# Kernel optimization log

Hardware: AMD Instinct MI355X
Metric: run time of the kernel (lower is better)

Reference implementation:

```python
import jax, jax.numpy as jnp
import numpy as np

BS, LX, LY, D, H, DK = 2, 2048, 2048, 1024, 16, 64


def setup_inputs() -> dict:
    key = jax.random.key(0)
    ks = jax.random.split(key, 12)
    s = 1.0 / np.sqrt(D)
    return {
        "x": jax.random.normal(ks[0], (BS, LX, D), jnp.float32),
        "y": jax.random.normal(ks[1], (BS, LY, D), jnp.float32),
        "mask": jnp.zeros((BS, 1, LX, LY), jnp.float32),
        "Wq": jax.random.normal(ks[2], (D, H * DK), jnp.float32) * s,
        "bq": jnp.zeros((H * DK,), jnp.float32),
        "Wk": jax.random.normal(ks[3], (D, H * DK), jnp.float32) * s,
        "bk": jnp.zeros((H * DK,), jnp.float32),
        "Wv": jax.random.normal(ks[4], (D, H * DK), jnp.float32) * s,
        "bv": jnp.zeros((H * DK,), jnp.float32),
        "Wo": jax.random.normal(ks[5], (H * DK, D), jnp.float32) * s,
        "bo": jnp.zeros((D,), jnp.float32),
    }


def reference(x, y, mask, Wq, bq, Wk, bk, Wv, bv, Wo, bo):
    bs, lx, _ = x.shape
    ly = y.shape[1]
    norm = DK ** 0.5
    # projections -> (bs, len, H, DK)
    q = (x @ Wq + bq).reshape(bs, lx, H, DK)
    k = (y @ Wk + bk).reshape(bs, ly, H, DK)
    v = (y @ Wv + bv).reshape(bs, ly, H, DK)
    # scores: (bs, H, lx, ly)
    scores = jnp.einsum('bxhd,byhd->bhxy', q, k) / norm + mask
    attn = jax.nn.softmax(scores, axis=-1)
    # output: (bs, lx, H, DK) -> (bs, lx, H*DK)
    out = jnp.einsum('bhxy,byhd->bxhd', attn, v).reshape(bs, lx, H * DK)
    return out @ Wo + bo
```

## Files before the change

kernel.cpp:

```cpp
#include <hip/hip_runtime.h>
#include <hip/hip_bf16.h>


typedef __bf16 bf16;
typedef __bf16 bf16x4 __attribute__((ext_vector_type(4)));
typedef __bf16 bf16x8 __attribute__((ext_vector_type(8)));
typedef float floatx4 __attribute__((ext_vector_type(4)));

#define MFMA16(a, b, c) __builtin_amdgcn_mfma_f32_16x16x32_bf16(a, b, c, 0, 0, 0)

constexpr int BS = 2, LX = 2048, LY = 2048, D = 1024, H = 16, DK = 64;
constexpr int HD = H * DK;
constexpr float LOG2E = 1.4426950408889634f;

__device__ __forceinline__ void cp16(const bf16* g, bf16* l) {
  __builtin_amdgcn_global_load_lds(
      (const __attribute__((address_space(1))) unsigned int*)g,
      (__attribute__((address_space(3))) unsigned int*)l, 16, 0, 0);
}

__global__ __launch_bounds__(256) void prep(const float* __restrict__ W0, bf16* __restrict__ T0,
                                            const float* __restrict__ W1, bf16* __restrict__ T1,
                                            const float* __restrict__ W2, bf16* __restrict__ T2,
                                            const float* __restrict__ W3, bf16* __restrict__ T3,
                                            const float* __restrict__ x, bf16* __restrict__ xb,
                                            const float* __restrict__ y, bf16* __restrict__ yb,
                                            const float* __restrict__ mask, int* __restrict__ flags) {
  const int id = blockIdx.x;
  const int t = threadIdx.x;
  if (id < 1024) {
    __shared__ bf16 tile[64][72];
    const float* W;
    bf16* T;
    switch (id >> 8) {
      case 0: W = W0; T = T0; break;
      case 1: W = W1; T = T1; break;
      case 2: W = W2; T = T2; break;
      default: W = W3; T = T3; break;
    }
    const int kt = id & 15, nt = (id >> 4) & 15;
    const int r = t >> 2, c4 = (t & 3) * 16;
    const float* src = W + (size_t)(kt * 64 + r) * 1024 + nt * 64 + c4;
#pragma unroll
    for (int i = 0; i < 16; i++) tile[r][c4 + i] = (bf16)src[i];
    __syncthreads();
    bf16 vals[16];
#pragma unroll
    for (int i = 0; i < 16; i++) vals[i] = tile[c4 + i][r];
    bf16* dst = T + (size_t)(nt * 64 + r) * 1024 + kt * 64 + c4;
#pragma unroll
    for (int i = 0; i < 16; i++) dst[i] = vals[i];
  } else if (id < 5120) {
    const int id2 = id - 1024;
    const float* src = (id2 >= 2048) ? y : x;
    bf16* dst = (id2 >= 2048) ? yb : xb;
    const size_t i = ((size_t)(id2 & 2047) * 256 + t) * 8;
    float4 a = *(const float4*)(src + i);
    float4 c = *(const float4*)(src + i + 4);
    bf16 tmp[8] = {(bf16)a.x, (bf16)a.y, (bf16)a.z, (bf16)a.w,
                   (bf16)c.x, (bf16)c.y, (bf16)c.z, (bf16)c.w};
    *(bf16x8*)(dst + i) = *(const bf16x8*)tmp;
  } else {
    const int id3 = id - 5120;
    const int region = id3 >> 5, sub = id3 & 31;
    const float4* p = (const float4*)mask + (size_t)region * 65536 + sub * 2048;
    bool nz = false;
#pragma unroll
    for (int it = 0; it < 8; it++) {
      float4 v = p[it * 256 + t];
      nz |= (v.x != 0.f) | (v.y != 0.f) | (v.z != 0.f) | (v.w != 0.f);
    }
    if (nz) atomicOr(&flags[region], 1);
  }
}

__global__ __launch_bounds__(512, 2) void qkv8(const bf16* __restrict__ xb, const bf16* __restrict__ yb,
                                               const bf16* __restrict__ Wtq, const bf16* __restrict__ Wtk,
                                               const bf16* __restrict__ Wtv,
                                               const float* __restrict__ bq, const float* __restrict__ bk,
                                               const float* __restrict__ bv,
                                               bf16* __restrict__ Qb, bf16* __restrict__ Kb,
                                               bf16* __restrict__ Vt) {
  constexpr int K = 1024, N = 1024;
  __shared__ __align__(16) bf16 As[2][2][128 * 64];
  __shared__ __align__(16) bf16 Bs[2][2][128 * 64];

  const int z = blockIdx.z;
  const bf16* A = (z == 0) ? xb : yb;
  const bf16* Bt = (z == 0) ? Wtq : (z == 1) ? Wtk : Wtv;
  const float* bias = (z == 0) ? bq : (z == 1) ? bk : bv;

  const int t = threadIdx.x;
  const int w = t >> 6, lane = t & 63, quad = lane >> 4, l15 = lane & 15;
  const int wm = w >> 2, wn = w & 3;
  const int mbase = blockIdx.y * 256, nbase = blockIdx.x * 256;
  const int srow = lane >> 3, schunk = (lane & 7) ^ srow;
  const int sx = quad ^ (l15 & 7);

  floatx4 acc[2][4][2][2] = {};
  bf16x8 af[4][2];
  bf16x8 bfr[2][2][2];

#define ST_A(ktt, half, slot)                                                                 \
  {                                                                                           \
    _Pragma("unroll") for (int j = 0; j < 2; j++) {                                           \
      const int r0 = w * 16 + j * 8;                                                          \
      cp16(A + (size_t)(mbase + (half) * 128 + r0 + srow) * K + (ktt) * 64 + schunk * 8,      \
           &As[slot][half][r0 * 64]);                                                         \
    }                                                                                         \
  }
#define ST_B(ktt, half, slot)                                                                 \
  {                                                                                           \
    _Pragma("unroll") for (int j = 0; j < 2; j++) {                                           \
      const int r0 = w * 16 + j * 8;                                                          \
      cp16(Bt + (size_t)(nbase + (half) * 128 + r0 + srow) * K + (ktt) * 64 + schunk * 8,     \
           &Bs[slot][half][r0 * 64]);                                                         \
    }                                                                                         \
  }
#define LOAD_A(slot, mh)                                                                      \
  {                                                                                           \
    _Pragma("unroll") for (int i = 0; i < 4; i++) {                                           \
      const bf16* p = &As[slot][mh][(wm * 64 + i * 16 + l15) * 64];                           \
      af[i][0] = *(const bf16x8*)(p + sx * 8);                                                \
      af[i][1] = *(const bf16x8*)(p + (sx ^ 4) * 8);                                          \
    }                                                                                         \
  }
#define LOAD_B(slot, nh)                                                                      \
  {                                                                                           \
    _Pragma("unroll") for (int j = 0; j < 2; j++) {                                           \
      const bf16* p = &Bs[slot][nh][(wn * 32 + j * 16 + l15) * 64];                           \
      bfr[nh][j][0] = *(const bf16x8*)(p + sx * 8);                                           \
      bfr[nh][j][1] = *(const bf16x8*)(p + (sx ^ 4) * 8);                                     \
    }                                                                                         \
  }
#define MFMA_Q(mh, nh)                                                                        \
  {                                                                                           \
    _Pragma("unroll") for (int i = 0; i < 4; i++)                                             \
        _Pragma("unroll") for (int j = 0; j < 2; j++) {                                       \
      acc[mh][i][nh][j] = MFMA16(af[i][0], bfr[nh][j][0], acc[mh][i][nh][j]);                 \
      acc[mh][i][nh][j] = MFMA16(af[i][1], bfr[nh][j][1], acc[mh][i][nh][j]);                 \
    }                                                                                         \
  }
#define BARX()                       \
  {                                  \
    asm volatile("" ::: "memory");   \
    __builtin_amdgcn_s_barrier();    \
    asm volatile("" ::: "memory");   \
  }
#define VMW(n) asm volatile("s_waitcnt vmcnt(" #n ")" ::: "memory")
#define LG0() asm volatile("s_waitcnt lgkmcnt(0)" ::: "memory")
#define NOPST {}
#define TILE_BODY(PAR, STG0, V0, STG1, V1, STG2, STG3, V3)  \
  {                                                         \
    LOAD_A(PAR, 0);                                         \
    LOAD_B(PAR, 0);                                         \
    STG0;                                                   \
    V0;                                                     \
    BARX();                                                 \
    LG0();                                                  \
    __builtin_amdgcn_s_setprio(1);                          \
    MFMA_Q(0, 0);                                           \
    __builtin_amdgcn_s_setprio(0);                          \
    BARX();                                                 \
    LOAD_B(PAR, 1);                                         \
    STG1;                                                   \
    V1;                                                     \
    BARX();                                                 \
    LG0();                                                  \
    __builtin_amdgcn_s_setprio(1);                          \
    MFMA_Q(0, 1);                                           \
    __builtin_amdgcn_s_setprio(0);                          \
    BARX();                                                 \
    LOAD_A(PAR, 1);                                         \
    STG2;                                                   \
    BARX();                                                 \
    LG0();                                                  \
    __builtin_amdgcn_s_setprio(1);                          \
    MFMA_Q(1, 0);                                           \
    __builtin_amdgcn_s_setprio(0);                          \
    BARX();                                                 \
    STG3;                                                   \
    V3;                                                     \
    BARX();                                                 \
    LG0();                                                  \
    __builtin_amdgcn_s_setprio(1);                          \
    MFMA_Q(1, 1);                                           \
    __builtin_amdgcn_s_setprio(0);                          \
    BARX();                                                 \
  }

  ST_A(0, 0, 0);
  ST_B(0, 0, 0);
  ST_B(0, 1, 0);
  ST_A(0, 1, 0);
  ST_A(1, 0, 1);
  ST_B(1, 0, 1);
  VMW(8);
  BARX();

#pragma unroll 1
  for (int kt = 0; kt < 14; kt += 2) {
    TILE_BODY(0, ST_B(kt + 1, 1, 1), VMW(8), ST_A(kt + 1, 1, 1), VMW(8),
              ST_A(kt + 2, 0, 0), ST_B(kt + 2, 0, 0), VMW(8));
    TILE_BODY(1, ST_B(kt + 2, 1, 0), VMW(8), ST_A(kt + 2, 1, 0), VMW(8),
              ST_A(kt + 3, 0, 1), ST_B(kt + 3, 0, 1), VMW(8));
  }
  TILE_BODY(0, ST_B(15, 1, 1), VMW(8), ST_A(15, 1, 1), VMW(8), NOPST, NOPST, VMW(4));
  TILE_BODY(1, NOPST, VMW(2), NOPST, VMW(0), NOPST, NOPST, NOPST);

#undef TILE_BODY
#undef NOPST
#undef LG0
#undef VMW
#undef BARX
#undef MFMA_Q
#undef LOAD_B
#undef LOAD_A
#undef ST_B
#undef ST_A

  if (z <= 1) {
    bf16* outp = (z == 0) ? Qb : Kb;
    const float sc = (z == 0) ? 0.125f * LOG2E : 1.0f;
#pragma unroll
    for (int nh = 0; nh < 2; nh++)
#pragma unroll
      for (int j = 0; j < 2; j++) {
        const int n = nbase + nh * 128 + wn * 32 + j * 16 + l15;
        const float bv2 = bias[n];
#pragma unroll
        for (int mh = 0; mh < 2; mh++)
#pragma unroll
          for (int i = 0; i < 4; i++)
#pragma unroll
            for (int r = 0; r < 4; r++) {
              const int m = mbase + mh * 128 + wm * 64 + i * 16 + quad * 4 + r;
              outp[(size_t)m * N + n] = (bf16)((acc[mh][i][nh][j][r] + bv2) * sc);
            }
      }
  } else {
    const int b = mbase >> 11;
    const int y0 = mbase & 2047;
#pragma unroll
    for (int nh = 0; nh < 2; nh++)
#pragma unroll
      for (int j = 0; j < 2; j++) {
        const int n = nbase + nh * 128 + wn * 32 + j * 16 + l15;
        const float bv2 = bias[n];
        const int hh = n >> 6, dk = n & 63;
        bf16* dst0 = Vt + ((size_t)(b * H + hh) * DK + dk) * LY + y0;
#pragma unroll
        for (int mh = 0; mh < 2; mh++)
#pragma unroll
          for (int i = 0; i < 4; i++) {
            const int yy = mh * 128 + wm * 64 + i * 16 + quad * 4;
            bf16 tmp[4];
#pragma unroll
            for (int r = 0; r < 4; r++) tmp[r] = (bf16)(acc[mh][i][nh][j][r] + bv2);
            *(bf16x4*)(dst0 + yy) = *(const bf16x4*)tmp;
          }
      }
  }
}

__global__ __launch_bounds__(256) void out_gemm(const bf16* __restrict__ A, const bf16* __restrict__ Bt,
                                                const float* __restrict__ bias, float* __restrict__ outp) {
  constexpr int K = 1024, N = 1024;
  __shared__ __align__(16) bf16 As[128 * 64];
  __shared__ __align__(16) bf16 Bs[64 * 64];
  const int t = threadIdx.x;
  const int w = t >> 6, lane = t & 63, quad = lane >> 4, l15 = lane & 15;
  const int mbase = blockIdx.y * 128, nbase = blockIdx.x * 64;
  const int srow = lane >> 3, schunk = (lane & 7) ^ srow;
  const int sx = quad ^ (l15 & 7);

  floatx4 acc[2][4] = {};
  for (int k0 = 0; k0 < K; k0 += 64) {
    __syncthreads();
#pragma unroll
    for (int j = 0; j < 4; j++) {
      const int r0 = w * 32 + j * 8;
      cp16(A + (size_t)(mbase + r0 + srow) * K + k0 + schunk * 8, As + r0 * 64);
    }
#pragma unroll
    for (int j = 0; j < 2; j++) {
      const int r0 = w * 16 + j * 8;
      cp16(Bt + (size_t)(nbase + r0 + srow) * K + k0 + schunk * 8, Bs + r0 * 64);
    }
    __syncthreads();
    bf16x8 af[2][2], bfr[4][2];
#pragma unroll
    for (int i = 0; i < 2; i++) {
      const int ra = w * 32 + i * 16 + l15;
      af[i][0] = *(const bf16x8*)&As[ra * 64 + sx * 8];
      af[i][1] = *(const bf16x8*)&As[ra * 64 + (sx ^ 4) * 8];
    }
#pragma unroll
    for (int jn = 0; jn < 4; jn++) {
      const int rb = jn * 16 + l15;
      bfr[jn][0] = *(const bf16x8*)&Bs[rb * 64 + sx * 8];
      bfr[jn][1] = *(const bf16x8*)&Bs[rb * 64 + (sx ^ 4) * 8];
    }
#pragma unroll
    for (int i = 0; i < 2; i++)
#pragma unroll
      for (int jn = 0; jn < 4; jn++) {
        acc[i][jn] = MFMA16(af[i][0], bfr[jn][0], acc[i][jn]);
        acc[i][jn] = MFMA16(af[i][1], bfr[jn][1], acc[i][jn]);
      }
  }
#pragma unroll
  for (int jn = 0; jn < 4; jn++) {
    const int n = nbase + jn * 16 + l15;
    const float bv2 = bias[n];
#pragma unroll
    for (int i = 0; i < 2; i++)
#pragma unroll
      for (int r = 0; r < 4; r++) {
        const int m = mbase + w * 32 + i * 16 + quad * 4 + r;
        outp[(size_t)m * N + n] = acc[i][jn][r] + bv2;
      }
  }
}

__global__ __launch_bounds__(256, 2) void attn8(const bf16* __restrict__ Q, const bf16* __restrict__ Kb,
                                                const bf16* __restrict__ Vt, const float* __restrict__ mask,
                                                const int* __restrict__ flags, bf16* __restrict__ Hout) {
  __shared__ __align__(16) bf16 Ks[2][64 * 64];
  __shared__ __align__(16) bf16 Vs[2][64 * 64];
  __shared__ __align__(16) bf16 Plds[4][32 * 72];
  const int t = threadIdx.x;
  const int w = t >> 6, lane = t & 63, quad = lane >> 4, l15 = lane & 15;
  const int xt = blockIdx.x, h = blockIdx.y, b = blockIdx.z;
  const int qbase = xt * 128 + w * 32;
  const int srow = lane >> 3, schunk = (lane & 7) ^ srow;
  const int sx = quad ^ (l15 & 7);

  bf16x8 qf[2][2];
#pragma unroll
  for (int rt = 0; rt < 2; rt++) {
    const bf16* qrow = Q + (size_t)(b * LX + qbase + rt * 16 + l15) * HD + h * DK;
    qf[rt][0] = *(const bf16x8*)(qrow + quad * 8);
    qf[rt][1] = *(const bf16x8*)(qrow + 32 + quad * 8);
  }
  const int mflag = flags[b * 16 + xt];

  bf16 onearr[8];
#pragma unroll
  for (int i = 0; i < 8; i++) onearr[i] = (bf16)((l15 == 0) ? 1.0f : 0.0f);
  const bf16x8 onesf = *(const bf16x8*)onearr;

  floatx4 o[2][4] = {};
  floatx4 ol[2] = {};

  const bf16* Kbase = Kb + (size_t)b * LY * HD + h * DK;
  const bf16* Vbase = Vt + (size_t)(b * H + h) * DK * LY;
  const float* mbase2 = mask + (size_t)(b * LX + qbase + l15) * LY;

#define STAGE(yt, bufi)                                                               \
  {                                                                                   \
    _Pragma("unroll") for (int j = 0; j < 2; j++) {                                   \
      const int r0 = w * 16 + j * 8;                                                  \
      cp16(Kbase + (size_t)((yt) + r0 + srow) * HD + schunk * 8, &Ks[bufi][r0 * 64]); \
      cp16(Vbase + (size_t)(r0 + srow) * LY + (yt) + schunk * 8, &Vs[bufi][r0 * 64]); \
    }                                                                                 \
  }

#define TILE(yt, BUF)                                                                       \
  {                                                                                         \
    const bf16* KsB = Ks[BUF];                                                              \
    const bf16* VsB = Vs[BUF];                                                              \
    bf16x8 kf[4][2];                                                                        \
    _Pragma("unroll") for (int nt = 0; nt < 4; nt++) {                                      \
      const int ry = nt * 16 + l15;                                                         \
      kf[nt][0] = *(const bf16x8*)&KsB[ry * 64 + sx * 8];                                   \
      kf[nt][1] = *(const bf16x8*)&KsB[ry * 64 + (sx ^ 4) * 8];                             \
    }                                                                                       \
    floatx4 s[2][4] = {};                                                                   \
    _Pragma("unroll") for (int nt = 0; nt < 4; nt++)                                        \
        _Pragma("unroll") for (int rt = 0; rt < 2; rt++) {                                  \
      s[rt][nt] = MFMA16(kf[nt][0], qf[rt][0], s[rt][nt]);                                  \
      s[rt][nt] = MFMA16(kf[nt][1], qf[rt][1], s[rt][nt]);                                  \
    }                                                                                       \
    if (mflag) {                                                                            \
      _Pragma("unroll") for (int rt = 0; rt < 2; rt++)                                      \
          _Pragma("unroll") for (int nt = 0; nt < 4; nt++) {                                \
        const float* mp = mbase2 + (size_t)rt * 16 * LY + (yt) + nt * 16 + quad * 4;        \
        float4 mv = *(const float4*)mp;                                                     \
        s[rt][nt][0] = fminf(s[rt][nt][0] + LOG2E * mv.x, 30.f);                            \
        s[rt][nt][1] = fminf(s[rt][nt][1] + LOG2E * mv.y, 30.f);                            \
        s[rt][nt][2] = fminf(s[rt][nt][2] + LOG2E * mv.z, 30.f);                            \
        s[rt][nt][3] = fminf(s[rt][nt][3] + LOG2E * mv.w, 30.f);                            \
      }                                                                                     \
    }                                                                                       \
    _Pragma("unroll") for (int rt = 0; rt < 2; rt++)                                        \
        _Pragma("unroll") for (int nt = 0; nt < 4; nt++) {                                  \
      bf16x4 pk;                                                                            \
      _Pragma("unroll") for (int r = 0; r < 4; r++)                                         \
          pk[r] = (bf16)__builtin_amdgcn_exp2f(s[rt][nt][r]);                               \
      *(bf16x4*)&Plds[w][(rt * 16 + l15) * 72 + nt * 16 + quad * 4] = pk;                   \
    }                                                                                       \
    bf16x8 pf[2][2];                                                                        \
    _Pragma("unroll") for (int rt = 0; rt < 2; rt++) {                                      \
      const bf16* prow = &Plds[w][(rt * 16 + l15) * 72];                                    \
      pf[rt][0] = *(const bf16x8*)(prow + quad * 8);                                        \
      pf[rt][1] = *(const bf16x8*)(prow + 32 + quad * 8);                                   \
    }                                                                                       \
    _Pragma("unroll") for (int u = 0; u < 4; u++) {                                         \
      const int rd = u * 16 + l15;                                                          \
      bf16x8 v0 = *(const bf16x8*)&VsB[rd * 64 + sx * 8];                                   \
      bf16x8 v1 = *(const bf16x8*)&VsB[rd * 64 + (sx ^ 4) * 8];                             \
      _Pragma("unroll") for (int rt = 0; rt < 2; rt++) {                                    \
        o[rt][u] = MFMA16(pf[rt][0], v0, o[rt][u]);                                         \
        o[rt][u] = MFMA16(pf[rt][1], v1, o[rt][u]);                                         \
      }                                                                                     \
    }                                                                                       \
    _Pragma("unroll") for (int rt = 0; rt < 2; rt++) {                                      \
      ol[rt] = MFMA16(pf[rt][0], onesf, ol[rt]);                                            \
      ol[rt] = MFMA16(pf[rt][1], onesf, ol[rt]);                                            \
    }                                                                                       \
  }

  STAGE(0, 0);
  for (int yt = 0; yt < LY; yt += 128) {
    __syncthreads();
    STAGE(yt + 64, 1);
    TILE(yt, 0);
    __syncthreads();
    if (yt + 128 < LY) STAGE(yt + 128, 0);
    TILE(yt + 64, 1);
  }

#pragma unroll
  for (int rt = 0; rt < 2; rt++)
#pragma unroll
    for (int r = 0; r < 4; r++) {
      const float lsum = __shfl(ol[rt][r], lane & 48, 64);
      const float rl = 1.0f / lsum;
      const int m = b * LX + qbase + rt * 16 + quad * 4 + r;
#pragma unroll
      for (int u = 0; u < 4; u++)
        Hout[(size_t)m * HD + h * DK + u * 16 + l15] = (bf16)(o[rt][u][r] * rl);
    }
#undef STAGE
#undef TILE
}

extern "C" void kernel_launch(void* const* d_in, const int* in_sizes, int n_in,
                              void* d_out, int out_size, void* d_ws, size_t ws_size,
                              hipStream_t stream) {
  const float* x = (const float*)d_in[0];
  const float* y = (const float*)d_in[1];
  const float* mask = (const float*)d_in[2];
  const float* Wq = (const float*)d_in[3];
  const float* bq = (const float*)d_in[4];
  const float* Wk = (const float*)d_in[5];
  const float* bk = (const float*)d_in[6];
  const float* Wv = (const float*)d_in[7];
  const float* bv = (const float*)d_in[8];
  const float* Wo = (const float*)d_in[9];
  const float* bo = (const float*)d_in[10];

  char* ws = (char*)d_ws;
  size_t off = 0;
  int* flags = (int*)(ws + off); off += 256;
  bf16* Qb = (bf16*)(ws + off); off += (size_t)BS * LX * HD * 2;
  bf16* Kb = (bf16*)(ws + off); off += (size_t)BS * LY * HD * 2;
  bf16* Vt = (bf16*)(ws + off); off += (size_t)BS * LY * HD * 2;
  bf16* Hb = (bf16*)(ws + off); off += (size_t)BS * LX * HD * 2;
  bf16* xbf = (bf16*)(ws + off); off += (size_t)BS * LX * D * 2;
  bf16* ybf = (bf16*)(ws + off); off += (size_t)BS * LY * D * 2;
  bf16* Wtq = (bf16*)(ws + off); off += (size_t)D * HD * 2;
  bf16* Wtk = (bf16*)(ws + off); off += (size_t)D * HD * 2;
  bf16* Wtv = (bf16*)(ws + off); off += (size_t)D * HD * 2;
  bf16* Wto = (bf16*)(ws + off); off += (size_t)HD * D * 2;

  dim3 blk(256);
  hipMemsetAsync(flags, 0, 32 * sizeof(int), stream);
  prep<<<dim3(6144), blk, 0, stream>>>(Wq, Wtq, Wk, Wtk, Wv, Wtv, Wo, Wto, x, xbf, y, ybf, mask, flags);
  qkv8<<<dim3(4, 16, 3), dim3(512), 0, stream>>>(xbf, ybf, Wtq, Wtk, Wtv, bq, bk, bv, Qb, Kb, Vt);
  attn8<<<dim3(16, 16, 2), blk, 0, stream>>>(Qb, Kb, Vt, mask, flags, Hb);
  out_gemm<<<dim3(16, 32), blk, 0, stream>>>(Hb, Wto, bo, (float*)d_out);
}
```

Measured before the change: 229.7 us.

## Software-pipeline attention tiles and keep P in registers via permlane swaps

```diff
diff --git a/kernel.cpp b/kernel.cpp
--- a/kernel.cpp
+++ b/kernel.cpp
@@ -3,9 +3,11 @@
 
 
 typedef __bf16 bf16;
+typedef __bf16 bf16x2 __attribute__((ext_vector_type(2)));
 typedef __bf16 bf16x4 __attribute__((ext_vector_type(4)));
 typedef __bf16 bf16x8 __attribute__((ext_vector_type(8)));
 typedef float floatx4 __attribute__((ext_vector_type(4)));
+typedef unsigned int uintx4 __attribute__((ext_vector_type(4)));
 
 #define MFMA16(a, b, c) __builtin_amdgcn_mfma_f32_16x16x32_bf16(a, b, c, 0, 0, 0)
 
@@ -17,6 +19,13 @@
   __builtin_amdgcn_global_load_lds(
       (const __attribute__((address_space(1))) unsigned int*)g,
       (__attribute__((address_space(3))) unsigned int*)l, 16, 0, 0);
+}
+
+__device__ __forceinline__ unsigned pk2(float a, float b) {
+  bf16x2 p;
+  p[0] = (bf16)a;
+  p[1] = (bf16)b;
+  return __builtin_bit_cast(unsigned, p);
 }
 
 __global__ __launch_bounds__(256) void prep(const float* __restrict__ W0, bf16* __restrict__ T0,
@@ -323,12 +332,11 @@
   }
 }
 
-__global__ __launch_bounds__(256, 2) void attn8(const bf16* __restrict__ Q, const bf16* __restrict__ Kb,
-                                                const bf16* __restrict__ Vt, const float* __restrict__ mask,
-                                                const int* __restrict__ flags, bf16* __restrict__ Hout) {
+__global__ __launch_bounds__(256, 2) void attn12(const bf16* __restrict__ Q, const bf16* __restrict__ Kb,
+                                                 const bf16* __restrict__ Vt, const float* __restrict__ mask,
+                                                 const int* __restrict__ flags, bf16* __restrict__ Hout) {
   __shared__ __align__(16) bf16 Ks[2][64 * 64];
   __shared__ __align__(16) bf16 Vs[2][64 * 64];
-  __shared__ __align__(16) bf16 Plds[4][32 * 72];
   const int t = threadIdx.x;
   const int w = t >> 6, lane = t & 63, quad = lane >> 4, l15 = lane & 15;
   const int xt = blockIdx.x, h = blockIdx.y, b = blockIdx.z;
@@ -352,6 +360,9 @@
 
   floatx4 o[2][4] = {};
   floatx4 ol[2] = {};
+  floatx4 s0[2][4], s1[2][4];
+  bf16x8 kf[4][2], vfA[4][2], vfB[4][2];
+  bf16x8 pf[2][2];
 
   const bf16* Kbase = Kb + (size_t)b * LY * HD + h * DK;
   const bf16* Vbase = Vt + (size_t)(b * H + h) * DK * LY;
@@ -365,71 +376,118 @@
       cp16(Vbase + (size_t)(r0 + srow) * LY + (yt) + schunk * 8, &Vs[bufi][r0 * 64]); \
     }                                                                                 \
   }
-
-#define TILE(yt, BUF)                                                                       \
-  {                                                                                         \
-    const bf16* KsB = Ks[BUF];                                                              \
-    const bf16* VsB = Vs[BUF];                                                              \
-    bf16x8 kf[4][2];                                                                        \
-    _Pragma("unroll") for (int nt = 0; nt < 4; nt++) {                                      \
-      const int ry = nt * 16 + l15;                                                         \
-      kf[nt][0] = *(const bf16x8*)&KsB[ry * 64 + sx * 8];                                   \
-      kf[nt][1] = *(const bf16x8*)&KsB[ry * 64 + (sx ^ 4) * 8];                             \
-    }                                                                                       \
-    floatx4 s[2][4] = {};                                                                   \
-    _Pragma("unroll") for (int nt = 0; nt < 4; nt++)                                        \
-        _Pragma("unroll") for (int rt = 0; rt < 2; rt++) {                                  \
-      s[rt][nt] = MFMA16(kf[nt][0], qf[rt][0], s[rt][nt]);                                  \
-      s[rt][nt] = MFMA16(kf[nt][1], qf[rt][1], s[rt][nt]);                                  \
-    }                                                                                       \
-    if (mflag) {                                                                            \
-      _Pragma("unroll") for (int rt = 0; rt < 2; rt++)                                      \
-          _Pragma("unroll") for (int nt = 0; nt < 4; nt++) {                                \
-        const float* mp = mbase2 + (size_t)rt * 16 * LY + (yt) + nt * 16 + quad * 4;        \
-        float4 mv = *(const float4*)mp;                                                     \
-        s[rt][nt][0] = fminf(s[rt][nt][0] + LOG2E * mv.x, 30.f);                            \
-        s[rt][nt][1] = fminf(s[rt][nt][1] + LOG2E * mv.y, 30.f);                            \
-        s[rt][nt][2] = fminf(s[rt][nt][2] + LOG2E * mv.z, 30.f);                            \
-        s[rt][nt][3] = fminf(s[rt][nt][3] + LOG2E * mv.w, 30.f);                            \
-      }                                                                                     \
-    }                                                                                       \
-    _Pragma("unroll") for (int rt = 0; rt < 2; rt++)                                        \
-        _Pragma("unroll") for (int nt = 0; nt < 4; nt++) {                                  \
-      bf16x4 pk;                                                                            \
-      _Pragma("unroll") for (int r = 0; r < 4; r++)                                         \
-          pk[r] = (bf16)__builtin_amdgcn_exp2f(s[rt][nt][r]);                               \
-      *(bf16x4*)&Plds[w][(rt * 16 + l15) * 72 + nt * 16 + quad * 4] = pk;                   \
-    }                                                                                       \
-    bf16x8 pf[2][2];                                                                        \
-    _Pragma("unroll") for (int rt = 0; rt < 2; rt++) {                                      \
-      const bf16* prow = &Plds[w][(rt * 16 + l15) * 72];                                    \
-      pf[rt][0] = *(const bf16x8*)(prow + quad * 8);                                        \
-      pf[rt][1] = *(const bf16x8*)(prow + 32 + quad * 8);                                   \
-    }                                                                                       \
-    _Pragma("unroll") for (int u = 0; u < 4; u++) {                                         \
-      const int rd = u * 16 + l15;                                                          \
-      bf16x8 v0 = *(const bf16x8*)&VsB[rd * 64 + sx * 8];                                   \
-      bf16x8 v1 = *(const bf16x8*)&VsB[rd * 64 + (sx ^ 4) * 8];                             \
-      _Pragma("unroll") for (int rt = 0; rt < 2; rt++) {                                    \
-        o[rt][u] = MFMA16(pf[rt][0], v0, o[rt][u]);                                         \
-        o[rt][u] = MFMA16(pf[rt][1], v1, o[rt][u]);                                         \
-      }                                                                                     \
-    }                                                                                       \
-    _Pragma("unroll") for (int rt = 0; rt < 2; rt++) {                                      \
-      ol[rt] = MFMA16(pf[rt][0], onesf, ol[rt]);                                            \
-      ol[rt] = MFMA16(pf[rt][1], onesf, ol[rt]);                                            \
-    }                                                                                       \
+#define KREAD(bufi)                                                                   \
+  {                                                                                   \
+    const bf16* KsB = Ks[bufi];                                                       \
+    _Pragma("unroll") for (int nt = 0; nt < 4; nt++) {                                \
+      const int ry = nt * 16 + l15;                                                   \
+      kf[nt][0] = *(const bf16x8*)&KsB[ry * 64 + sx * 8];                             \
+      kf[nt][1] = *(const bf16x8*)&KsB[ry * 64 + (sx ^ 4) * 8];                       \
+    }                                                                                 \
+  }
+#define VREAD(bufi, VF)                                                               \
+  {                                                                                   \
+    const bf16* VsB = Vs[bufi];                                                       \
+    _Pragma("unroll") for (int u = 0; u < 4; u++) {                                   \
+      const int rd = u * 16 + l15;                                                    \
+      VF[u][0] = *(const bf16x8*)&VsB[rd * 64 + sx * 8];                              \
+      VF[u][1] = *(const bf16x8*)&VsB[rd * 64 + (sx ^ 4) * 8];                        \
+    }                                                                                 \
+  }
+#define SCOMP(SD)                                                                     \
+  {                                                                                   \
+    __builtin_amdgcn_s_setprio(1);                                                    \
+    _Pragma("unroll") for (int nt = 0; nt < 4; nt++)                                  \
+        _Pragma("unroll") for (int rt = 0; rt < 2; rt++) {                            \
+      floatx4 sz = {0.f, 0.f, 0.f, 0.f};                                              \
+      sz = MFMA16(kf[nt][0], qf[rt][0], sz);                                          \
+      SD[rt][nt] = MFMA16(kf[nt][1], qf[rt][1], sz);                                  \
+    }                                                                                 \
+    __builtin_amdgcn_s_setprio(0);                                                    \
+  }
+#define EXPP(SS, yt)                                                                  \
+  {                                                                                   \
+    if (mflag) {                                                                      \
+      _Pragma("unroll") for (int rt = 0; rt < 2; rt++)                                \
+          _Pragma("unroll") for (int nt = 0; nt < 4; nt++) {                          \
+        const float* mp = mbase2 + (size_t)rt * 16 * LY + (yt) + nt * 16 + quad * 4;  \
+        float4 mv = *(const float4*)mp;                                               \
+        SS[rt][nt][0] = fminf(SS[rt][nt][0] + LOG2E * mv.x, 30.f);                    \
+        SS[rt][nt][1] = fminf(SS[rt][nt][1] + LOG2E * mv.y, 30.f);                    \
+        SS[rt][nt][2] = fminf(SS[rt][nt][2] + LOG2E * mv.z, 30.f);                    \
+        SS[rt][nt][3] = fminf(SS[rt][nt][3] + LOG2E * mv.w, 30.f);                    \
+      }                                                                               \
+    }                                                                                 \
+    _Pragma("unroll") for (int rt = 0; rt < 2; rt++) {                                \
+      uintx4 wd0, wd1;                                                                \
+      _Pragma("unroll") for (int F = 0; F < 2; F++)                                   \
+          _Pragma("unroll") for (int hh = 0; hh < 2; hh++) {                          \
+        unsigned wa = pk2(__builtin_amdgcn_exp2f(SS[rt][2 * F][2 * hh]),              \
+                          __builtin_amdgcn_exp2f(SS[rt][2 * F][2 * hh + 1]));         \
+        unsigned wb = pk2(__builtin_amdgcn_exp2f(SS[rt][2 * F + 1][2 * hh]),          \
+                          __builtin_amdgcn_exp2f(SS[rt][2 * F + 1][2 * hh + 1]));     \
+        asm("v_permlane32_swap_b32 %0, %1" : "+v"(wa), "+v"(wb));                     \
+        asm("v_permlane16_swap_b32 %0, %1" : "+v"(wa), "+v"(wb));                     \
+        if (F == 0) {                                                                 \
+          wd0[hh] = wa;                                                               \
+          wd0[hh + 2] = wb;                                                           \
+        } else {                                                                      \
+          wd1[hh] = wa;                                                               \
+          wd1[hh + 2] = wb;                                                           \
+        }                                                                             \
+      }                                                                               \
+      pf[rt][0] = __builtin_bit_cast(bf16x8, wd0);                                    \
+      pf[rt][1] = __builtin_bit_cast(bf16x8, wd1);                                    \
+    }                                                                                 \
+  }
+#define PVC(VF)                                                                       \
+  {                                                                                   \
+    __builtin_amdgcn_s_setprio(1);                                                    \
+    _Pragma("unroll") for (int u = 0; u < 4; u++) {                                   \
+      _Pragma("unroll") for (int rt = 0; rt < 2; rt++) {                              \
+        o[rt][u] = MFMA16(pf[rt][0], VF[u][0], o[rt][u]);                             \
+        o[rt][u] = MFMA16(pf[rt][1], VF[u][1], o[rt][u]);                             \
+      }                                                                               \
+    }                                                                                 \
+    _Pragma("unroll") for (int rt = 0; rt < 2; rt++) {                                \
+      ol[rt] = MFMA16(pf[rt][0], onesf, ol[rt]);                                      \
+      ol[rt] = MFMA16(pf[rt][1], onesf, ol[rt]);                                      \
+    }                                                                                 \
+    __builtin_amdgcn_s_setprio(0);                                                    \
   }
 
   STAGE(0, 0);
-  for (int yt = 0; yt < LY; yt += 128) {
+  __syncthreads();
+  STAGE(64, 1);
+  KREAD(0);
+  SCOMP(s0);
+  VREAD(0, vfA);
+
+#pragma unroll 1
+  for (int i = 1; i < 31; i += 2) {
     __syncthreads();
-    STAGE(yt + 64, 1);
-    TILE(yt, 0);
+    STAGE((i + 1) * 64, 0);
+    KREAD(1);
+    SCOMP(s1);
+    VREAD(1, vfB);
+    EXPP(s0, (i - 1) * 64);
+    PVC(vfA);
     __syncthreads();
-    if (yt + 128 < LY) STAGE(yt + 128, 0);
-    TILE(yt + 64, 1);
-  }
+    if (i + 2 < 32) STAGE((i + 2) * 64, 1);
+    KREAD(0);
+    SCOMP(s0);
+    VREAD(0, vfA);
+    EXPP(s1, i * 64);
+    PVC(vfB);
+  }
+  __syncthreads();
+  KREAD(1);
+  SCOMP(s1);
+  VREAD(1, vfB);
+  EXPP(s0, 30 * 64);
+  PVC(vfA);
+  EXPP(s1, 31 * 64);
+  PVC(vfB);
 
 #pragma unroll
   for (int rt = 0; rt < 2; rt++)
@@ -443,7 +501,11 @@
         Hout[(size_t)m * HD + h * DK + u * 16 + l15] = (bf16)(o[rt][u][r] * rl);
     }
 #undef STAGE
-#undef TILE
+#undef KREAD
+#undef VREAD
+#undef SCOMP
+#undef EXPP
+#undef PVC
 }
 
 extern "C" void kernel_launch(void* const* d_in, const int* in_sizes, int n_in,
@@ -479,6 +541,6 @@
   hipMemsetAsync(flags, 0, 32 * sizeof(int), stream);
   prep<<<dim3(6144), blk, 0, stream>>>(Wq, Wtq, Wk, Wtk, Wv, Wtv, Wo, Wto, x, xbf, y, ybf, mask, flags);
   qkv8<<<dim3(4, 16, 3), dim3(512), 0, stream>>>(xbf, ybf, Wtq, Wtk, Wtv, bq, bk, bv, Qb, Kb, Vt);
-  attn8<<<dim3(16, 16, 2), blk, 0, stream>>>(Qb, Kb, Vt, mask, flags, Hb);
+  attn12<<<dim3(16, 16, 2), blk, 0, stream>>>(Qb, Kb, Vt, mask, flags, Hb);
   out_gemm<<<dim3(16, 32), blk, 0, stream>>>(Hb, Wto, bo, (float*)d_out);
 }
```

After: 223.5 us, median of 2. -2.7%, faster.
